# Kernel optimization log

Hardware: AMD Instinct MI355X
Metric: run time of the kernel (lower is better)

Reference implementation:

```python
import jax, jax.numpy as jnp
import numpy as np

N_POINTS = 1_200_000
MAX_POINTS = 10
MAX_VOXELS = 160_000


def setup_inputs() -> dict:
    key = jax.random.key(0)
    k1, k2, k3 = jax.random.split(key, 3)
    xy = jax.random.normal(k1, (N_POINTS, 2), dtype=jnp.float32) * 18.0
    z = jax.random.normal(k2, (N_POINTS, 1), dtype=jnp.float32) * 1.3 - 1.0
    feat = jax.random.normal(k3, (N_POINTS, 2), dtype=jnp.float32)
    points = jnp.concatenate([xy, z, feat], axis=1)
    return {
        'points': points,
        'voxel_size': jnp.array([0.075, 0.075, 0.2], dtype=jnp.float32),
        'coors_range': jnp.array([-54.0, -54.0, -5.0, 54.0, 54.0, 3.0], dtype=jnp.float32),
        'max_points': MAX_POINTS,
        'max_voxels': MAX_VOXELS,
    }


def reference(points, voxel_size, coors_range, max_points, max_voxels):
    """Deterministic hard voxelization (mmcv hard_voxelize semantics):
    - quantize points to integer voxel coords, drop out-of-range points
    - voxels are numbered in order of first point appearance
    - at most `max_points` points per voxel (first ones kept, in point order)
    - at most `max_voxels` voxels (first ones kept)
    Returns fixed-shape buffers plus voxel_num (original slices to voxel_num).
    """
    N, C = points.shape
    vmin = coors_range[:3]
    grid = jnp.round((coors_range[3:] - vmin) / voxel_size).astype(jnp.int32)  # (gx, gy, gz)

    c = jnp.floor((points[:, :3] - vmin) / voxel_size).astype(jnp.int32)  # [N,3] xyz voxel coords
    valid = jnp.all((c >= 0) & (c < grid), axis=1)

    gx, gy, gz = grid[0].astype(jnp.int64), grid[1].astype(jnp.int64), grid[2].astype(jnp.int64)
    lin = (c[:, 0].astype(jnp.int64) * gy + c[:, 1].astype(jnp.int64)) * gz + c[:, 2].astype(jnp.int64)
    total = gx * gy * gz
    lin = jnp.where(valid, lin, total)  # sentinel sorts last

    idx = jnp.arange(N, dtype=jnp.int64)
    # composite key: group by voxel, original point order within each voxel
    order = jnp.argsort(lin * N + idx)  # [N] stable grouping
    lin_s = lin[order]
    valid_s = valid[order]

    is_head = valid_s & jnp.concatenate([jnp.array([True]), lin_s[1:] != lin_s[:-1]])
    pos = jnp.arange(N, dtype=jnp.int32)
    head_pos = jax.lax.cummax(jnp.where(is_head, pos, -1))  # head position of each point's group
    slot = pos - head_pos  # slot within voxel (point order)

    # voxel id = rank of the group's first point among all group-head original indices
    head_orig = jnp.where(is_head, order, N)  # sentinel N for non-heads
    rank = jnp.argsort(jnp.argsort(head_orig)).astype(jnp.int32)  # heads -> 0..H-1 in first-occurrence order
    vox_id = rank[head_pos]  # [N] voxel id per sorted point

    keep = valid_s & (slot < max_points) & (vox_id < max_voxels)
    vid = jnp.where(keep, vox_id, max_voxels)  # dump row for dropped points
    slt = jnp.where(keep, slot, 0)
    vals = jnp.where(keep[:, None], points[order], 0.0)

    voxels = jnp.zeros((max_voxels + 1, max_points, C), dtype=points.dtype)
    voxels = voxels.at[vid, slt].add(vals)[:max_voxels]

    # coors in (z, y, x) order as in mmcv
    c_rev = c[order][:, ::-1]
    vid_h = jnp.where(is_head & (rank < max_voxels), rank, max_voxels)
    coors = jnp.zeros((max_voxels + 1, 3), dtype=jnp.int32)
    coors = coors.at[vid_h].set(jnp.where((vid_h < max_voxels)[:, None], c_rev, 0))[:max_voxels]

    cnt_idx = jnp.where(valid_s & (vox_id < max_voxels), vox_id, max_voxels)
    counts = jnp.zeros((max_voxels + 1,), dtype=jnp.int32).at[cnt_idx].add(1)[:max_voxels]
    num_points_per_voxel = jnp.minimum(counts, max_points)

    voxel_num = jnp.minimum(is_head.sum(dtype=jnp.int32), max_voxels)
    return voxels, coors, num_points_per_voxel, voxel_num
```

## Files before the change

### kernel.cpp

```cpp
#include <hip/hip_runtime.h>
#include <cstdint>

static constexpr int C     = 5;
static constexpr int MAXP  = 10;
static constexpr int MAXV  = 160000;
static constexpr int BLK   = 256;
static constexpr int RB    = 2048;
static constexpr int BCAP  = 1024;
static constexpr int EPT   = 8;
static constexpr int ELEMS = BLK * EPT;

static constexpr int VOX_OFF = 0;
static constexpr int CO_OFF  = MAXV * MAXP * C;
static constexpr int NPV_OFF = CO_OFF + MAXV * 3;
static constexpr int VN_OFF  = NPV_OFF + MAXV;

typedef unsigned long long u64;
static constexpr u64 BYTEMUL = 0x0101010101010101ull;

__device__ __forceinline__ int hashb(int k) {
    return (int)(((uint32_t)k * 2654435761u) >> 21);
}

__global__ void vx_prep(const float* __restrict__ pts, const float* __restrict__ vsz,
                        const float* __restrict__ crg, int* __restrict__ key0,
                        int* __restrict__ hist, u64* __restrict__ flags8,
                        int* __restrict__ ctrl, float* __restrict__ out,
                        int NP, int NP8) {
    __shared__ int sh[RB];
    int t = threadIdx.x, b = blockIdx.x;
    for (int d = t; d < RB; d += BLK) sh[d] = 0;
    if (b == 0 && t < 8) ctrl[t] = 0;
    float vx = vsz[0], vy = vsz[1], vz = vsz[2];
    float x0 = crg[0], y0 = crg[1], z0 = crg[2];
    int gx = (int)rintf((crg[3] - x0) / vx);
    int gy = (int)rintf((crg[4] - y0) / vy);
    int gz = (int)rintf((crg[5] - z0) / vz);
    __syncthreads();
    int base = b * ELEMS;
    #pragma unroll
    for (int r = 0; r < EPT; r++) {
        int i = base + r * BLK + t;
        if (i < NP) {
            float px = pts[i * C], py = pts[i * C + 1], pz = pts[i * C + 2];
            int cx = (int)floorf((px - x0) / vx);
            int cy = (int)floorf((py - y0) / vy);
            int cz = (int)floorf((pz - z0) / vz);
            bool valid = (cx >= 0) & (cx < gx) & (cy >= 0) & (cy < gy) & (cz >= 0) & (cz < gz);
            int k = (cx * gy + cy) * gz + cz;
            key0[i] = valid ? k : -1;
            if (valid) atomicAdd(&sh[hashb(k)], 1);
        }
    }
    __syncthreads();
    for (int d = t; d < RB; d += BLK) hist[b * RB + d] = sh[d];
    int tid = b * BLK + t, nth = gridDim.x * BLK;
    float4* co4 = (float4*)(out + CO_OFF);
    const float4 z4 = make_float4(0.f, 0.f, 0.f, 0.f);
    const int nco4 = (VN_OFF - CO_OFF) / 4;
    for (int i = tid; i < nco4; i += nth) co4[i] = z4;
    for (int i = tid; i < NP8; i += nth) flags8[i] = 0ull;
}

__global__ void vx_scanw(int* __restrict__ hist, int* __restrict__ dtot, int NB) {
    int t = threadIdx.x;
    int lane = t & 63;
    int d = blockIdx.x * 4 + (t >> 6);
    int carry = 0;
    for (int base = 0; base < NB; base += 64) {
        int b = base + lane;
        int v = (b < NB) ? hist[b * RB + d] : 0;
        int x = v;
        #pragma unroll
        for (int o = 1; o < 64; o <<= 1) {
            int y = __shfl_up(x, o, 64);
            if (lane >= o) x += y;
        }
        if (b < NB) hist[b * RB + d] = carry + x - v;
        carry += __shfl(x, 63, 64);
    }
    if (lane == 0) dtot[d] = carry;
}

__global__ void vx_scat(const int* __restrict__ key0, const int* __restrict__ hist,
                        const int* __restrict__ dtot, u64* __restrict__ pairA,
                        int* __restrict__ ctrl, int NP) {
    __shared__ int cnt[RB];
    __shared__ int svld;
    int t = threadIdx.x, b = blockIdx.x;
    int lane = t & 63;
    if (t == 0) svld = 0;
    if (t < 64) {
        int loc[32]; int run = 0;
        #pragma unroll
        for (int j = 0; j < 32; j++) { loc[j] = run; run += dtot[t * 32 + j]; }
        int tot = run;
        for (int o = 1; o < 64; o <<= 1) {
            int x = __shfl_up(tot, o, 64);
            if (lane >= o) tot += x;
        }
        int excl = tot - run;
        #pragma unroll
        for (int j = 0; j < 32; j++) cnt[t * 32 + j] = excl + loc[j];
    }
    __syncthreads();
    for (int d = t; d < RB; d += BLK) cnt[d] += hist[b * RB + d];
    __syncthreads();
    int base = b * ELEMS;
    int myv = 0;
    #pragma unroll
    for (int r = 0; r < EPT; r++) {
        int i = base + r * BLK + t;
        if (i < NP) {
            int k = key0[i];
            if (k >= 0) {
                int pos = atomicAdd(&cnt[hashb(k)], 1);
                pairA[pos] = ((u64)(uint32_t)k << 32) | (uint32_t)i;
                myv++;
            }
        }
    }
    atomicAdd(&svld, myv);
    __syncthreads();
    if (t == 0) atomicAdd(&ctrl[1], svld);
}

__global__ void __launch_bounds__(512) vx_group(const u64* __restrict__ pairA,
                                                const int* __restrict__ dtot,
                                                u64* __restrict__ flags8,
                                                uint4* __restrict__ recs) {
    __shared__ int htab[BCAP];
    __shared__ int cnt[BCAP];
    __shared__ int seg[BCAP];
    __shared__ u64 sq[BCAP];
    __shared__ int swp[8];
    __shared__ int sb[2];
    int t = threadIdx.x, d = blockIdx.x;
    if (t < 64) {
        int acc = 0;
        for (int j = t; j < d; j += 64) acc += dtot[j];
        #pragma unroll
        for (int o = 32; o > 0; o >>= 1) acc += __shfl_down(acc, o, 64);
        if (t == 0) { sb[0] = acc; sb[1] = dtot[d]; }
    }
    for (int i = t; i < BCAP; i += 512) { htab[i] = -1; cnt[i] = 0; }
    __syncthreads();
    int start = sb[0], size = sb[1];
    if (size <= 0) return;
    if (size > BCAP) size = BCAP;
    bool a0 = t < size, a1 = t + 512 < size;
    u64 e0 = a0 ? pairA[start + t] : 0;
    u64 e1 = a1 ? pairA[start + 512 + t] : 0;
    int k0 = (int)(e0 >> 32), k1 = (int)(e1 >> 32);
    int s0 = 0, s1 = 0;
    if (a0) {
        s0 = (int)(((uint32_t)k0 * 0x85EBCA77u) >> 22);
        for (int it = 0; it < BCAP; ++it) {
            int old = atomicCAS(&htab[s0], -1, k0);
            if (old == -1 || old == k0) break;
            s0 = (s0 + 1) & (BCAP - 1);
        }
        atomicAdd(&cnt[s0], 1);
    }
    if (a1) {
        s1 = (int)(((uint32_t)k1 * 0x85EBCA77u) >> 22);
        for (int it = 0; it < BCAP; ++it) {
            int old = atomicCAS(&htab[s1], -1, k1);
            if (old == -1 || old == k1) break;
            s1 = (s1 + 1) & (BCAP - 1);
        }
        atomicAdd(&cnt[s1], 1);
    }
    __syncthreads();
    int c0 = cnt[2 * t], c1 = cnt[2 * t + 1];
    int v = c0 + c1;
    int lane = t & 63, wv = t >> 6;
    int x = v;
    #pragma unroll
    for (int o = 1; o < 64; o <<= 1) {
        int y = __shfl_up(x, o, 64);
        if (lane >= o) x += y;
    }
    if (lane == 63) swp[wv] = x;
    for (int i = t; i < BCAP; i += 512) htab[i] = 0;
    __syncthreads();
    if (t == 0) {
        int acc = 0;
        #pragma unroll
        for (int j = 0; j < 8; j++) { int tmp = swp[j]; swp[j] = acc; acc += tmp; }
    }
    __syncthreads();
    int excl = swp[wv] + x - v;
    seg[2 * t] = excl;
    seg[2 * t + 1] = excl + c0;
    __syncthreads();
    int st0 = 0, cn0 = 0, st1 = 0, cn1 = 0;
    if (a0) { st0 = seg[s0]; cn0 = cnt[s0]; if (cn0 > 1) sq[st0 + atomicAdd(&htab[s0], 1)] = e0; }
    if (a1) { st1 = seg[s1]; cn1 = cnt[s1]; if (cn1 > 1) sq[st1 + atomicAdd(&htab[s1], 1)] = e1; }
    __syncthreads();
    int r0 = 0, r1 = 0;
    if (a0 && cn0 > 1) {
        uint32_t my = (uint32_t)e0;
        for (int q = st0; q < st0 + cn0; q++) r0 += ((uint32_t)sq[q] < my);
        if (r0 == 0) htab[s0] = (int)my;
    }
    if (a1 && cn1 > 1) {
        uint32_t my = (uint32_t)e1;
        for (int q = st1; q < st1 + cn1; q++) r1 += ((uint32_t)sq[q] < my);
        if (r1 == 0) htab[s1] = (int)my;
    }
    __syncthreads();
    unsigned char* flags = (unsigned char*)flags8;
    if (a0) {
        uint32_t my = (uint32_t)e0;
        uint32_t head = (cn0 > 1) ? (uint32_t)htab[s0] : my;
        if (r0 == 0) flags[my] = 1;
        recs[start + st0 + r0] =
            make_uint4((uint32_t)k0, my, head, (uint32_t)r0 | ((uint32_t)cn0 << 16));
    }
    if (a1) {
        uint32_t my = (uint32_t)e1;
        uint32_t head = (cn1 > 1) ? (uint32_t)htab[s1] : my;
        if (r1 == 0) flags[my] = 1;
        recs[start + st1 + r1] =
            make_uint4((uint32_t)k1, my, head, (uint32_t)r1 | ((uint32_t)cn1 << 16));
    }
}

__global__ void vx_wpA(const u64* __restrict__ flags8, int* __restrict__ wsum, int NP8) {
    __shared__ int s[BLK];
    int t = threadIdx.x, i = blockIdx.x * BLK + t;
    u64 wv = (i < NP8) ? flags8[i] : 0ull;
    s[t] = (int)((wv * BYTEMUL) >> 56);
    __syncthreads();
    for (int o = BLK / 2; o > 0; o >>= 1) { if (t < o) s[t] += s[t + o]; __syncthreads(); }
    if (t == 0) wsum[blockIdx.x] = s[0];
}

__global__ void vx_wp2(const u64* __restrict__ flags8, const int* __restrict__ wsum,
                       int* __restrict__ wpfx, int* __restrict__ ctrl,
                       float* __restrict__ out_vnum, int NP8) {
    __shared__ int s[BLK];
    __shared__ int eS;
    int t = threadIdx.x, b = blockIdx.x;
    if (t < 64) {
        int acc = 0;
        for (int base = 0; base < b; base += 64) {
            int idx = base + t;
            int v = (idx < b) ? wsum[idx] : 0;
            #pragma unroll
            for (int o = 32; o > 0; o >>= 1) v += __shfl_down(v, o, 64);
            acc += v;
        }
        if (t == 0) eS = acc;
    }
    int i = b * BLK + t;
    u64 wv = (i < NP8) ? flags8[i] : 0ull;
    int v = (int)((wv * BYTEMUL) >> 56);
    s[t] = v;
    __syncthreads();
    for (int o = 1; o < BLK; o <<= 1) {
        int x = (t >= o) ? s[t - o] : 0; __syncthreads();
        s[t] += x; __syncthreads();
    }
    if (i < NP8) wpfx[i] = eS + s[t] - v;
    if (b == gridDim.x - 1 && t == BLK - 1) {
        int G = eS + s[t];
        int Gk = G < MAXV ? G : MAXV;
        ctrl[0] = Gk;
        out_vnum[0] = (float)Gk;
    }
}

__device__ __forceinline__ int vox_rank(const u64* flags8, const int* wpfx, int io) {
    int w = io >> 3, b8 = io & 7;
    u64 below = flags8[w] & ((1ull << (8 * b8)) - 1ull);
    return wpfx[w] + (int)((below * BYTEMUL) >> 56);
}

__global__ void vx_final(const uint4* __restrict__ recs, const u64* __restrict__ flags8,
                         const int* __restrict__ wpfx, const int* __restrict__ ctrl,
                         const float* __restrict__ pts, const float* __restrict__ vsz,
                         const float* __restrict__ crg, float* __restrict__ out, int NP) {
    int t = threadIdx.x, b = blockIdx.x;
    int nval = ctrl[1], Gk = ctrl[0];
    int gyd = (int)rintf((crg[4] - crg[1]) / vsz[1]);
    int gzd = (int)rintf((crg[5] - crg[2]) / vsz[2]);
    int base = b * ELEMS;
    #pragma unroll
    for (int r = 0; r < EPT; r++) {
        int i = base + r * BLK + t;
        if (i >= nval) continue;
        uint4 rec = recs[i];
        int k = (int)rec.x;
        uint32_t my = rec.y, head = rec.z;
        int slot = (int)(rec.w & 0xFFFFu);
        int gsz  = (int)(rec.w >> 16);
        if (slot >= MAXP || head >= (uint32_t)NP || my >= (uint32_t)NP) continue;
        int vid = vox_rank(flags8, wpfx, (int)head);
        if (vid >= MAXV) continue;
        const float* src = pts + my * C;
        float* dst = out + (vid * MAXP + slot) * C;
        dst[0] = src[0]; dst[1] = src[1]; dst[2] = src[2]; dst[3] = src[3]; dst[4] = src[4];
        if (slot == 0) {
            int cz = k % gzd; int rr = k / gzd; int cy = rr % gyd; int cx = rr / gyd;
            out[CO_OFF + vid * 3 + 0] = (float)cz;
            out[CO_OFF + vid * 3 + 1] = (float)cy;
            out[CO_OFF + vid * 3 + 2] = (float)cx;
            int np = gsz < MAXP ? gsz : MAXP;
            out[NPV_OFF + vid] = (float)np;
            float* rowz = out + (vid * MAXP + np) * C;
            int nz = (MAXP - np) * C;
            for (int z = 0; z < nz; z++) rowz[z] = 0.f;
        }
    }
    int nz2 = (MAXV - Gk) * (MAXP * C) / 2;
    if (nz2 > 0) {
        float2* z2 = (float2*)(out + Gk * MAXP * C);
        const float2 zz = make_float2(0.f, 0.f);
        int tid = b * BLK + t, nth = gridDim.x * BLK;
        for (int i = tid; i < nz2; i += nth) z2[i] = zz;
    }
}

extern "C" void kernel_launch(void* const* d_in, const int* in_sizes, int n_in,
                              void* d_out, int out_size, void* d_ws, size_t ws_size,
                              hipStream_t stream) {
    if (!d_out || !d_ws || n_in < 3) return;
    const float* pts = (const float*)d_in[0];
    const float* vsz = (const float*)d_in[1];
    const float* crg = (const float*)d_in[2];
    if (!pts || !vsz || !crg) return;
    const int NP  = in_sizes[0] / C;
    if (NP <= 0) return;
    const int NB  = (NP + ELEMS - 1) / ELEMS;
    const int NP8 = (NP + 7) / 8;
    const int NWB = (NP8 + BLK - 1) / BLK;

    size_t need = (size_t)NP * 8ull
                + (size_t)NP * 16ull
                + (size_t)NP * 4ull
                + (size_t)RB * NB * 4ull
                + (size_t)RB * 4ull
                + (size_t)NP8 * 8ull
                + (size_t)NP8 * 4ull
                + (size_t)NWB * 4ull + 64ull;
    if (ws_size < need) return;
    if ((size_t)out_size < (size_t)VN_OFF + 1) return;

    u64*   pairA  = (u64*)d_ws;
    uint4* recs   = (uint4*)(pairA + NP);
    int*   key0   = (int*)(recs + NP);
    int*   hist   = key0 + NP;
    int*   dtot   = hist + (size_t)RB * NB;
    u64*   flags8 = (u64*)(dtot + RB);
    int*   wpfx   = (int*)(flags8 + NP8);
    int*   wsum   = wpfx + NP8;
    int*   ctrl   = wsum + NWB;
    float* out    = (float*)d_out;

    vx_prep<<<NB, BLK, 0, stream>>>(pts, vsz, crg, key0, hist, flags8, ctrl, out, NP, NP8);
    vx_scanw<<<RB / 4, BLK, 0, stream>>>(hist, dtot, NB);
    vx_scat<<<NB, BLK, 0, stream>>>(key0, hist, dtot, pairA, ctrl, NP);
    vx_group<<<RB, 512, 0, stream>>>(pairA, dtot, flags8, recs);
    vx_wpA<<<NWB, BLK, 0, stream>>>(flags8, wsum, NP8);
    vx_wp2<<<NWB, BLK, 0, stream>>>(flags8, wsum, wpfx, ctrl, out + VN_OFF, NP8);
    vx_final<<<NB, BLK, 0, stream>>>(recs, flags8, wpfx, ctrl, pts, vsz, crg, out, NP);
}
```

Before: 203.0 us.

## Pack group records into 64 bits and zero whole output upfront

Group records shrink from 16-byte uint4 to packed 64-bit words, with a head flag, the key and group size for heads, and the head index and slot for the rest. This halves record write and read traffic between the grouping and final kernels. The whole output buffer is now zeroed with float4 stores in the prep kernel, replacing per-voxel tail zeroing and the tail fill in the final kernel. The final kernel launches more blocks with fewer elements per thread. The cost is zeroing the full voxel buffer, including rows that are later overwritten, and a new limit of NP below 2^25.

```diff
diff --git a/kernel.cpp b/kernel.cpp
--- a/kernel.cpp
+++ b/kernel.cpp
@@ -17,6 +17,7 @@
 
 typedef unsigned long long u64;
 static constexpr u64 BYTEMUL = 0x0101010101010101ull;
+
 
 __device__ __forceinline__ int hashb(int k) {
     return (int)(((uint32_t)k * 2654435761u) >> 21);
@@ -55,10 +56,9 @@
     __syncthreads();
     for (int d = t; d < RB; d += BLK) hist[b * RB + d] = sh[d];
     int tid = b * BLK + t, nth = gridDim.x * BLK;
-    float4* co4 = (float4*)(out + CO_OFF);
+    float4* out4 = (float4*)out;
     const float4 z4 = make_float4(0.f, 0.f, 0.f, 0.f);
-    const int nco4 = (VN_OFF - CO_OFF) / 4;
-    for (int i = tid; i < nco4; i += nth) co4[i] = z4;
+    for (int i = tid; i < VN_OFF / 4; i += nth) out4[i] = z4;
     for (int i = tid; i < NP8; i += nth) flags8[i] = 0ull;
 }
 
@@ -128,7 +128,7 @@
 __global__ void __launch_bounds__(512) vx_group(const u64* __restrict__ pairA,
                                                 const int* __restrict__ dtot,
                                                 u64* __restrict__ flags8,
-                                                uint4* __restrict__ recs) {
+                                                u64* __restrict__ recs) {
     __shared__ int htab[BCAP];
     __shared__ int cnt[BCAP];
     __shared__ int seg[BCAP];
@@ -213,17 +213,31 @@
     unsigned char* flags = (unsigned char*)flags8;
     if (a0) {
         uint32_t my = (uint32_t)e0;
-        uint32_t head = (cn0 > 1) ? (uint32_t)htab[s0] : my;
-        if (r0 == 0) flags[my] = 1;
-        recs[start + st0 + r0] =
-            make_uint4((uint32_t)k0, my, head, (uint32_t)r0 | ((uint32_t)cn0 << 16));
+        u64 rec;
+        if (r0 == 0) {
+            flags[my] = 1;
+            int g = cn0 < 15 ? cn0 : 15;
+            rec = (1ull << 63) | ((u64)g << 52) | ((u64)(uint32_t)k0 << 25) | my;
+        } else {
+            uint32_t head = (uint32_t)htab[s0];
+            int sl = r0 < 15 ? r0 : 15;
+            rec = ((u64)sl << 50) | ((u64)head << 25) | my;
+        }
+        recs[start + st0 + r0] = rec;
     }
     if (a1) {
         uint32_t my = (uint32_t)e1;
-        uint32_t head = (cn1 > 1) ? (uint32_t)htab[s1] : my;
-        if (r1 == 0) flags[my] = 1;
-        recs[start + st1 + r1] =
-            make_uint4((uint32_t)k1, my, head, (uint32_t)r1 | ((uint32_t)cn1 << 16));
+        u64 rec;
+        if (r1 == 0) {
+            flags[my] = 1;
+            int g = cn1 < 15 ? cn1 : 15;
+            rec = (1ull << 63) | ((u64)g << 52) | ((u64)(uint32_t)k1 << 25) | my;
+        } else {
+            uint32_t head = (uint32_t)htab[s1];
+            int sl = r1 < 15 ? r1 : 15;
+            rec = ((u64)sl << 50) | ((u64)head << 25) | my;
+        }
+        recs[start + st1 + r1] = rec;
     }
 }
 
@@ -238,8 +252,7 @@
 }
 
 __global__ void vx_wp2(const u64* __restrict__ flags8, const int* __restrict__ wsum,
-                       int* __restrict__ wpfx, int* __restrict__ ctrl,
-                       float* __restrict__ out_vnum, int NP8) {
+                       int* __restrict__ wpfx, float* __restrict__ out_vnum, int NP8) {
     __shared__ int s[BLK];
     __shared__ int eS;
     int t = threadIdx.x, b = blockIdx.x;
@@ -266,9 +279,7 @@
     if (i < NP8) wpfx[i] = eS + s[t] - v;
     if (b == gridDim.x - 1 && t == BLK - 1) {
         int G = eS + s[t];
-        int Gk = G < MAXV ? G : MAXV;
-        ctrl[0] = Gk;
-        out_vnum[0] = (float)Gk;
+        out_vnum[0] = (float)(G < MAXV ? G : MAXV);
     }
 }
 
@@ -278,48 +289,46 @@
     return wpfx[w] + (int)((below * BYTEMUL) >> 56);
 }
 
-__global__ void vx_final(const uint4* __restrict__ recs, const u64* __restrict__ flags8,
+static constexpr int EPTF = 2;
+__global__ void vx_final(const u64* __restrict__ recs, const u64* __restrict__ flags8,
                          const int* __restrict__ wpfx, const int* __restrict__ ctrl,
                          const float* __restrict__ pts, const float* __restrict__ vsz,
                          const float* __restrict__ crg, float* __restrict__ out, int NP) {
     int t = threadIdx.x, b = blockIdx.x;
-    int nval = ctrl[1], Gk = ctrl[0];
+    int nval = ctrl[1];
     int gyd = (int)rintf((crg[4] - crg[1]) / vsz[1]);
     int gzd = (int)rintf((crg[5] - crg[2]) / vsz[2]);
-    int base = b * ELEMS;
+    int base = b * (BLK * EPTF);
     #pragma unroll
-    for (int r = 0; r < EPT; r++) {
+    for (int r = 0; r < EPTF; r++) {
         int i = base + r * BLK + t;
         if (i >= nval) continue;
-        uint4 rec = recs[i];
-        int k = (int)rec.x;
-        uint32_t my = rec.y, head = rec.z;
-        int slot = (int)(rec.w & 0xFFFFu);
-        int gsz  = (int)(rec.w >> 16);
-        if (slot >= MAXP || head >= (uint32_t)NP || my >= (uint32_t)NP) continue;
+        u64 rec = recs[i];
+        uint32_t my = (uint32_t)(rec & 0x1FFFFFFu);
+        bool ishead = (rec >> 63) != 0;
+        uint32_t head;
+        int slot, k = 0, gsz = 0;
+        if (ishead) {
+            head = my; slot = 0;
+            k = (int)((rec >> 25) & 0x7FFFFFFu);
+            gsz = (int)((rec >> 52) & 15u);
+        } else {
+            head = (uint32_t)((rec >> 25) & 0x1FFFFFFu);
+            slot = (int)((rec >> 50) & 15u);
+        }
+        if (slot >= MAXP || my >= (uint32_t)NP || head >= (uint32_t)NP) continue;
         int vid = vox_rank(flags8, wpfx, (int)head);
         if (vid >= MAXV) continue;
         const float* src = pts + my * C;
         float* dst = out + (vid * MAXP + slot) * C;
         dst[0] = src[0]; dst[1] = src[1]; dst[2] = src[2]; dst[3] = src[3]; dst[4] = src[4];
-        if (slot == 0) {
+        if (ishead) {
             int cz = k % gzd; int rr = k / gzd; int cy = rr % gyd; int cx = rr / gyd;
             out[CO_OFF + vid * 3 + 0] = (float)cz;
             out[CO_OFF + vid * 3 + 1] = (float)cy;
             out[CO_OFF + vid * 3 + 2] = (float)cx;
-            int np = gsz < MAXP ? gsz : MAXP;
-            out[NPV_OFF + vid] = (float)np;
-            float* rowz = out + (vid * MAXP + np) * C;
-            int nz = (MAXP - np) * C;
-            for (int z = 0; z < nz; z++) rowz[z] = 0.f;
-        }
-    }
-    int nz2 = (MAXV - Gk) * (MAXP * C) / 2;
-    if (nz2 > 0) {
-        float2* z2 = (float2*)(out + Gk * MAXP * C);
-        const float2 zz = make_float2(0.f, 0.f);
-        int tid = b * BLK + t, nth = gridDim.x * BLK;
-        for (int i = tid; i < nz2; i += nth) z2[i] = zz;
+            out[NPV_OFF + vid] = (float)(gsz < MAXP ? gsz : MAXP);
+        }
     }
 }
 
@@ -332,13 +341,14 @@
     const float* crg = (const float*)d_in[2];
     if (!pts || !vsz || !crg) return;
     const int NP  = in_sizes[0] / C;
-    if (NP <= 0) return;
+    if (NP <= 0 || NP >= (1 << 25)) return;
     const int NB  = (NP + ELEMS - 1) / ELEMS;
     const int NP8 = (NP + 7) / 8;
     const int NWB = (NP8 + BLK - 1) / BLK;
+    const int NBF = (NP + BLK * EPTF - 1) / (BLK * EPTF);
 
     size_t need = (size_t)NP * 8ull
-                + (size_t)NP * 16ull
+                + (size_t)NP * 8ull
                 + (size_t)NP * 4ull
                 + (size_t)RB * NB * 4ull
                 + (size_t)RB * 4ull
@@ -349,7 +359,7 @@
     if ((size_t)out_size < (size_t)VN_OFF + 1) return;
 
     u64*   pairA  = (u64*)d_ws;
-    uint4* recs   = (uint4*)(pairA + NP);
+    u64*   recs   = pairA + NP;
     int*   key0   = (int*)(recs + NP);
     int*   hist   = key0 + NP;
     int*   dtot   = hist + (size_t)RB * NB;
@@ -364,6 +374,6 @@
     vx_scat<<<NB, BLK, 0, stream>>>(key0, hist, dtot, pairA, ctrl, NP);
     vx_group<<<RB, 512, 0, stream>>>(pairA, dtot, flags8, recs);
     vx_wpA<<<NWB, BLK, 0, stream>>>(flags8, wsum, NP8);
-    vx_wp2<<<NWB, BLK, 0, stream>>>(flags8, wsum, wpfx, ctrl, out + VN_OFF, NP8);
-    vx_final<<<NB, BLK, 0, stream>>>(recs, flags8, wpfx, ctrl, pts, vsz, crg, out, NP);
-}
+    vx_wp2<<<NWB, BLK, 0, stream>>>(flags8, wsum, wpfx, out + VN_OFF, NP8);
+    vx_final<<<NBF, BLK, 0, stream>>>(recs, flags8, wpfx, ctrl, pts, vsz, crg, out, NP);
+}
```

Result: faster. 179.3 us (-11.7%).
